# Kernel optimization log

Measured on AMD Instinct MI355X. Metric: run time of the kernel, lower is better.

Reference implementation:

```python
import jax, jax.numpy as jnp
import numpy as np

B, N, D = 8, 500, 256
H, W = 480, 640
NUM_CORNERS = 500
MATCH_RADIUS = 1.0
SCORE_RADIUS = 8
BETA = (1.0, 1.0, 1.0)


def _rodrigues(aa):
    theta = jnp.linalg.norm(aa, axis=-1, keepdims=True)
    k = aa / jnp.maximum(theta, 1e-8)
    kx, ky, kz = k[..., 0], k[..., 1], k[..., 2]
    z = jnp.zeros_like(kx)
    Km = jnp.stack([jnp.stack([z, -kz, ky], -1),
                    jnp.stack([kz, z, -kx], -1),
                    jnp.stack([-ky, kx, z], -1)], -2)
    th = theta[..., None]
    return jnp.eye(3) + jnp.sin(th) * Km + (1. - jnp.cos(th)) * (Km @ Km)


def setup_inputs() -> dict:
    key = jax.random.key(0)
    ks = jax.random.split(key, 8)
    descriptors = jax.random.normal(ks[0], (B, N, D), jnp.float32)
    points = jax.random.uniform(ks[1], (B, N, 2), jnp.float32, -1.0, 1.0)
    pointness = jax.random.uniform(ks[2], (B, 1, H, W), jnp.float32) * 0.98 + 0.01
    depths_dense = jax.random.uniform(ks[3], (B, 1, H, W), jnp.float32) * 4.0 + 1.0
    imgs = jax.random.uniform(ks[4], (B, 3, H, W), jnp.float32)
    aa = jax.random.normal(ks[5], (B, 3), jnp.float32) * 0.02
    t = jax.random.normal(ks[6], (B, 3), jnp.float32) * 0.05
    R = _rodrigues(aa)
    poses = jnp.tile(jnp.eye(4, dtype=jnp.float32), (B, 1, 1))
    poses = poses.at[:, :3, :3].set(R).at[:, :3, 3].set(t)
    Kmat = jnp.tile(jnp.array([[300., 0., W / 2.], [0., 300., H / 2.], [0., 0., 1.]], jnp.float32), (B, 1, 1))
    return {"descriptors": descriptors, "points": points, "pointness": pointness,
            "depths_dense": depths_dense, "poses": poses, "K": Kmat, "imgs": imgs}


def denormalize(pts, h, w):
    return jnp.stack([(pts[..., 0] + 1.) * 0.5 * (w - 1), (pts[..., 1] + 1.) * 0.5 * (h - 1)], -1)


def normalize_pix(pts, h, w):
    return jnp.stack([2. * pts[..., 0] / (w - 1) - 1., 2. * pts[..., 1] / (h - 1) - 1.], -1)


def bilinear_sample(img, px):  # img (H,W), px (...,2) pixel coords
    x = jnp.clip(px[..., 0], 0., W - 1.)
    y = jnp.clip(px[..., 1], 0., H - 1.)
    x0 = jnp.floor(x); y0 = jnp.floor(y)
    x1 = jnp.minimum(x0 + 1., W - 1.); y1 = jnp.minimum(y0 + 1., H - 1.)
    wx = x - x0; wy = y - y0
    x0i = x0.astype(jnp.int32); x1i = x1.astype(jnp.int32)
    y0i = y0.astype(jnp.int32); y1i = y1.astype(jnp.int32)
    v00 = img[y0i, x0i]; v01 = img[y0i, x1i]
    v10 = img[y1i, x0i]; v11 = img[y1i, x1i]
    return v00 * (1 - wx) * (1 - wy) + v01 * wx * (1 - wy) + v10 * (1 - wx) * wy + v11 * wx * wy


def pairwise_project(pts, depths, poses, Kmat):
    # pts (B,N,2) normalized; proj[i,j] = points of frame i projected into frame j
    px = denormalize(pts, H, W)
    d = jax.vmap(bilinear_sample)(depths[:, 0], px)  # (B,Np)
    Kinv = jnp.linalg.inv(Kmat)
    homog = jnp.concatenate([px, jnp.ones_like(px[..., :1])], -1)
    Xc = d[..., None] * jnp.einsum('bij,bnj->bni', Kinv, homog)
    Rm = poses[:, :3, :3]; t = poses[:, :3, 3]
    Xw = jnp.einsum('bij,bnj->bni', Rm, Xc) + t[:, None, :]
    diff = Xw[:, None, :, :] - t[None, :, None, :]           # (src,dst,Np,3)
    Xj = jnp.einsum('jba,ijnb->ijna', Rm, diff)              # R_j^T (Xw - t_j)
    uvw = jnp.einsum('jab,ijnb->ijna', Kmat, Xj)
    z = uvw[..., 2]
    zs = jnp.where(jnp.abs(z) < 1e-6, 1e-6, z)
    pn = normalize_pix(jnp.stack([uvw[..., 0] / zs, uvw[..., 1] / zs], -1), H, W)
    invis = (z <= 1e-6) | (jnp.abs(pn[..., 0]) > 1.) | (jnp.abs(pn[..., 1]) > 1.) | (d[:, None, :] <= 0.)
    return pn, invis


def conv2d_same(x, k):
    return jax.lax.conv_general_dilated(x, k[None, None].astype(x.dtype), (1, 1), 'SAME')


_SOBEL_X = np.array([[-1, 0, 1], [-2, 0, 2], [-1, 0, 1]], np.float32) / 8.


def _gauss_kernel(size=7, sigma=1.0):
    r = np.arange(size) - size // 2
    g = np.exp(-r ** 2 / (2 * sigma ** 2)); g /= g.sum()
    return np.outer(g, g).astype(np.float32)


_GAUSS = _gauss_kernel()


def gftt_response(gray):  # min-eigenvalue (Shi-Tomasi) corner response
    gx = conv2d_same(gray, jnp.asarray(_SOBEL_X))
    gy = conv2d_same(gray, jnp.asarray(_SOBEL_X.T))
    g = jnp.asarray(_GAUSS)
    dx2 = conv2d_same(gx * gx, g)
    dy2 = conv2d_same(gy * gy, g)
    dxy = conv2d_same(gx * gy, g)
    tr = dx2 + dy2
    det = dx2 * dy2 - dxy * dxy
    return 0.5 * (tr - jnp.sqrt(jnp.clip(tr * tr - 4. * det, 0.)))


def nms2d(x, k=5):
    mp = jax.lax.reduce_window(x, -jnp.inf, jax.lax.max, (1, 1, k, k), (1, 1, 1, 1), 'SAME')
    return x * (x == mp).astype(x.dtype)


def get_corners(imgs, depths, poses, Kmat):
    gray = (0.299 * imgs[:, 0] + 0.587 * imgs[:, 1] + 0.114 * imgs[:, 2])[:, None]
    c = nms2d(gftt_response(gray))
    r = SCORE_RADIUS
    blocks = c.reshape(B, 1, H // r, r, W // r, r)  # unfold/fold with stride==kernel
    bm = blocks.max(axis=(3, 5), keepdims=True)
    blocks = blocks * ((blocks > 0) & (blocks == bm)).astype(c.dtype)
    c = blocks.reshape(B, 1, H, W)
    vals, idx = jax.lax.top_k(c.reshape(B, -1), NUM_CORNERS)
    xs = (idx % W).astype(jnp.float32)
    ys = (idx // W).astype(jnp.float32)
    coords = normalize_pix(jnp.stack([xs, ys], -1), H, W)
    proj, invis = pairwise_project(coords, depths, poses, Kmat)
    proj = jnp.where(invis[..., None], -2.0, proj)
    combined = jnp.transpose(proj, (1, 0, 2, 3)).reshape(B, B * NUM_CORNERS, 2)  # per dst frame
    pix = jnp.round(denormalize(combined, H, W)).astype(jnp.int32)
    wq, hq = pix[..., 0], pix[..., 1]
    valid = wq >= 0
    v = jnp.tile(vals.reshape(-1), B).reshape(B, B * NUM_CORNERS)
    v = jnp.where(valid, v, 0.)
    hc = jnp.clip(hq, 0, H - 1)
    wc = jnp.clip(wq, 0, W - 1)
    bidx = jnp.broadcast_to(jnp.arange(B)[:, None], (B, B * NUM_CORNERS))
    target = jnp.zeros((B, H, W), imgs.dtype).at[bidx, hc, wc].max(v)
    target = nms2d(target[:, None])
    return (target > 0).astype(imgs.dtype)


def distinction_loss(desc):
    dn = desc / jnp.clip(jnp.linalg.norm(desc, axis=-1, keepdims=True), 1e-8)
    c = jnp.einsum('bnd,bmd->bnm', dn, dn)
    return jax.nn.relu(c).mean()


def match_loss(desc, points, proj, invis):
    p_src = denormalize(jax.lax.stop_gradient(points), H, W)  # (B,N,2)
    p_dst = denormalize(jax.lax.stop_gradient(proj), H, W)    # (src a, dst b, N, 2)
    diff = p_src[None, :, :, None, :] - p_dst[:, :, None, :, :]  # (a,b,n,m,2)
    m = (diff ** 2).sum(-1) <= MATCH_RADIUS ** 2
    m = m & (~invis)[:, :, :, None]                 # zero invisible rows
    n_idx = jnp.arange(N)
    m = m & (n_idx[:, None] < n_idx[None, :])       # triu(diagonal=1)
    dn = desc / jnp.clip(jnp.linalg.norm(desc, axis=-1, keepdims=True), 1e-8)
    cos = jnp.einsum('bnd,amd->abnm', dn, dn)       # cosine(desc[b,n], desc[a,m])
    mf = m.astype(desc.dtype)
    cnt = jnp.maximum(mf.sum(), 1.)
    return ((1. - cos) * mf).sum() / cnt


def bce(p, t):
    logp = jnp.maximum(jnp.log(p), -100.)
    log1p = jnp.maximum(jnp.log(1. - p), -100.)
    return -(t * logp + (1. - t) * log1p).mean()


def reference(descriptors, points, pointness, depths_dense, poses, K, imgs):
    distinction = distinction_loss(descriptors)
    target = get_corners(imgs, depths_dense, poses, K)
    cornerness = bce(pointness, target)
    proj, invis = pairwise_project(points, depths_dense, poses, K)
    match = match_loss(descriptors, points, proj, invis)
    return BETA[0] * distinction + BETA[1] * cornerness + BETA[2] * match
```

## Files before the change

kernel.cpp:

```cpp
#include <hip/hip_runtime.h>
#include <math.h>

#define BB 8
#define NN 500
#define DDIM 256
#define HH 480
#define WW 640
#define HWSZ (HH*WW)
#define BHW (BB*HWSZ)
#define NBLK 4800
#define NOVF 3392
#define NLIST (BB*NN*BB)
#define NBCE2 512
#define NCORR 125
#define NDM 66

#define PD_DIST  0
#define PD_MS    512
#define PD_MC    1024
#define PD_BCE   1536
#define PD_CORR  2560
#define PD_TOTAL 2688

typedef __attribute__((ext_vector_type(8))) short short8;
typedef __attribute__((ext_vector_type(4))) float f32x4;


static __device__ __forceinline__ float wredmaxf(float v) {
  #pragma unroll
  for (int o = 1; o < 64; o <<= 1) v = fmaxf(v, __shfl_xor(v, o, 64));
  return v;
}

static __device__ __forceinline__ double blockRedSum256(double v) {
  __shared__ double sp[4];
  __syncthreads();
  #pragma unroll
  for (int o = 32; o > 0; o >>= 1) v += __shfl_down(v, o, 64);
  int lane = threadIdx.x & 63, wid = threadIdx.x >> 6;
  if (lane == 0) sp[wid] = v;
  __syncthreads();
  double r = 0.0;
  if (threadIdx.x == 0) r = sp[0] + sp[1] + sp[2] + sp[3];
  return r;
}

static __device__ __forceinline__ unsigned short f2bf(float f) {
  unsigned u = __float_as_uint(f);
  return (unsigned short)((u + 0x7FFFu + ((u >> 16) & 1u)) >> 16);
}

static __device__ __forceinline__ float bilin(const float* __restrict__ img, float px, float py) {
  float x = fminf(fmaxf(px, 0.0f), 639.0f);
  float y = fminf(fmaxf(py, 0.0f), 479.0f);
  float x0 = floorf(x), y0 = floorf(y);
  float x1 = fminf(x0 + 1.0f, 639.0f);
  float y1 = fminf(y0 + 1.0f, 479.0f);
  float wx = x - x0, wy = y - y0;
  int x0i = (int)x0, x1i = (int)x1, y0i = (int)y0, y1i = (int)y1;
  float v00 = img[y0i*WW + x0i], v01 = img[y0i*WW + x1i];
  float v10 = img[y1i*WW + x0i], v11 = img[y1i*WW + x1i];
  return v00*(1.0f-wx)*(1.0f-wy) + v01*wx*(1.0f-wy) + v10*(1.0f-wx)*wy + v11*wx*wy;
}

static __device__ void src_compute(float px, float py, const float* __restrict__ dep,
                                   const float* __restrict__ poses, const float* __restrict__ Km,
                                   int bimg, float* Xw, float* dout) {
  float d = bilin(dep, px, py);
  const float* Kb = Km + bimg*9;
  double a00=Kb[0],a01=Kb[1],a02=Kb[2],a10=Kb[3],a11=Kb[4],a12=Kb[5],a20=Kb[6],a21=Kb[7],a22=Kb[8];
  double det = a00*(a11*a22-a12*a21) - a01*(a10*a22-a12*a20) + a02*(a10*a21-a11*a20);
  double id = 1.0/det;
  float i00=(float)((a11*a22-a12*a21)*id), i01=(float)((a02*a21-a01*a22)*id), i02=(float)((a01*a12-a02*a11)*id);
  float i10=(float)((a12*a20-a10*a22)*id), i11=(float)((a00*a22-a02*a20)*id), i12=(float)((a02*a10-a00*a12)*id);
  float i20=(float)((a10*a21-a11*a20)*id), i21=(float)((a01*a20-a00*a21)*id), i22=(float)((a00*a11-a01*a10)*id);
  float c0 = i00*px + i01*py + i02;
  float c1 = i10*px + i11*py + i12;
  float c2 = i20*px + i21*py + i22;
  float X0 = d*c0, X1 = d*c1, X2 = d*c2;
  const float* P = poses + bimg*16;
  Xw[0] = (P[0]*X0 + P[1]*X1 + P[2]*X2)  + P[3];
  Xw[1] = (P[4]*X0 + P[5]*X1 + P[6]*X2)  + P[7];
  Xw[2] = (P[8]*X0 + P[9]*X1 + P[10]*X2) + P[11];
  *dout = d;
}

static __device__ void project_to(const float* __restrict__ poses, const float* __restrict__ Km,
                                  int j, const float* Xw, float dsrc,
                                  float* pnx, float* pny, bool* invis) {
  const float* P = poses + j*16;
  float d0 = Xw[0]-P[3], d1 = Xw[1]-P[7], d2 = Xw[2]-P[11];
  float Xj0 = P[0]*d0 + P[4]*d1 + P[8]*d2;
  float Xj1 = P[1]*d0 + P[5]*d1 + P[9]*d2;
  float Xj2 = P[2]*d0 + P[6]*d1 + P[10]*d2;
  const float* Kb = Km + j*9;
  float u = Kb[0]*Xj0 + Kb[1]*Xj1 + Kb[2]*Xj2;
  float v = Kb[3]*Xj0 + Kb[4]*Xj1 + Kb[5]*Xj2;
  float z = Kb[6]*Xj0 + Kb[7]*Xj1 + Kb[8]*Xj2;
  float zs = (fabsf(z) < 1e-6f) ? 1e-6f : z;
  float pu = u/zs, pv = v/zs;
  float nx = 2.0f*pu/639.0f - 1.0f;
  float ny = 2.0f*pv/479.0f - 1.0f;
  *pnx = nx; *pny = ny;
  *invis = (z <= 1e-6f) || (fabsf(nx) > 1.0f) || (fabsf(ny) > 1.0f) || (dsrc <= 0.0f);
}


__global__ __launch_bounds__(256) void k_gfused(const float* __restrict__ imgs, float* __restrict__ resp,
                                                int* __restrict__ ovf, int* __restrict__ list,
                                                unsigned int* __restrict__ dnb_u) {
  __shared__ float smem[6536];
  __shared__ float Gw[7];
  float* sgxy = smem;
  float* gray = smem + 2888;
  float* hxx  = smem + 2888;
  float* hyy  = hxx + 1216;
  float* hxy  = hyy + 1216;
  int bx = blockIdx.x*32, by = blockIdx.y*32, b = blockIdx.z;
  int tid = threadIdx.x;
  if (blockIdx.z == 0 && blockIdx.y == 0) {
    int g = blockIdx.x*256 + tid;
    for (int e = g; e < BB*64; e += 20*256) ovf[e] = 0;
    for (int e = g; e < NLIST; e += 20*256) list[e] = -1;
    for (int e = g; e < 12288; e += 20*256) {
      int bi = e / 1536, r = e % 1536;
      dnb_u[(bi*512 + 500)*128 + r] = 0u;
    }
  }
  if (tid < 7) {
    double g[7]; double s = 0.0;
    for (int q = 0; q < 7; q++) { double r = (double)(q-3); g[q] = exp(-(r*r)/2.0); s += g[q]; }
    Gw[tid] = (float)(g[tid]/s);
  }
  const float* ib = imgs + (size_t)b*3*HWSZ;
  for (int e = tid; e < 40*40; e += 256) {
    int ly = e/40, lx = e%40;
    int X = bx - 4 + lx, Y = by - 4 + ly;
    float v = 0.f;
    if (X>=0 && X<WW && Y>=0 && Y<HH) {
      int p = Y*WW + X;
      v = 0.299f*ib[p] + 0.587f*ib[HWSZ+p] + 0.114f*ib[2*HWSZ+p];
    }
    gray[ly*41+lx] = v;
  }
  __syncthreads();
  const float kxw[3][3] = {{-0.125f,0.f,0.125f},{-0.25f,0.f,0.25f},{-0.125f,0.f,0.125f}};
  for (int e = tid; e < 38*38; e += 256) {
    int rr = e/38, c = e%38;
    int X = bx - 3 + c, Y = by - 3 + rr;
    float sx = 0.f, sy = 0.f;
    #pragma unroll
    for (int i = 0; i < 3; i++)
      #pragma unroll
      for (int j = 0; j < 3; j++) {
        float v = gray[(rr+i)*41 + (c+j)];
        sx += kxw[i][j]*v;
        sy += kxw[j][i]*v;
      }
    bool in = (X>=0 && X<WW && Y>=0 && Y<HH);
    sgxy[e*2]   = in ? sx : 0.f;
    sgxy[e*2+1] = in ? sy : 0.f;
  }
  __syncthreads();
  for (int e = tid; e < 38*32; e += 256) {
    int rr = e >> 5, co = e & 31;
    int base = (rr*38 + co)*2;
    float axx = 0.f, ayy = 0.f, axy = 0.f;
    #pragma unroll
    for (int j = 0; j < 7; j++) {
      float a = sgxy[base + j*2];
      float c = sgxy[base + j*2 + 1];
      float Gj = Gw[j];
      axx += Gj*(a*a); ayy += Gj*(c*c); axy += Gj*(a*c);
    }
    hxx[e] = axx; hyy[e] = ayy; hxy[e] = axy;
  }
  __syncthreads();
  int tx = tid & 31, ty = tid >> 5;
  int r0 = ty*4;
  float axx[4] = {0,0,0,0}, ayy[4] = {0,0,0,0}, axy[4] = {0,0,0,0};
  #pragma unroll
  for (int rr = 0; rr < 10; rr++) {
    int r = r0 + rr;
    float vxx = hxx[r*32+tx], vyy = hyy[r*32+tx], vxy = hxy[r*32+tx];
    #pragma unroll
    for (int o = 0; o < 4; o++) {
      int i = rr - o;
      if (i >= 0 && i <= 6) {
        float Gi = Gw[i];
        axx[o] += Gi*vxx; ayy[o] += Gi*vyy; axy[o] += Gi*vxy;
      }
    }
  }
  #pragma unroll
  for (int o = 0; o < 4; o++) {
    float tr = axx[o] + ayy[o];
    float det = axx[o]*ayy[o] - axy[o]*axy[o];
    float disc = fmaxf(tr*tr - 4.0f*det, 0.f);
    int y = by + r0 + o;
    resp[(size_t)b*HWSZ + y*WW + (bx+tx)] = 0.5f*(tr - sqrtf(disc));
  }
}

__global__ __launch_bounds__(256) void k_nmscand(const float* __restrict__ resp, float* __restrict__ cv,
                          int* __restrict__ ci, float* __restrict__ cvo,
                          int* __restrict__ cio, int* __restrict__ ovf,
                          float* __restrict__ target) {
  __shared__ float s[36*37];
  __shared__ float hm[36*32];
  __shared__ float c32[32*32];
  int bx = blockIdx.x*32, by = blockIdx.y*32, b = blockIdx.z;
  int tid = threadIdx.x;
  const float* r = resp + (size_t)b*HWSZ;
  for (int e = tid; e < 36*36; e += 256) {
    int ly = e/36, lx = e%36;
    int X = bx - 2 + lx, Y = by - 2 + ly;
    s[ly*37+lx] = (X>=0 && X<WW && Y>=0 && Y<HH) ? r[Y*WW+X] : -INFINITY;
  }
  __syncthreads();
  for (int e = tid; e < 36*32; e += 256) {
    int rr = e >> 5, co = e & 31;
    int base = rr*37 + co;
    float m = s[base];
    m = fmaxf(m, s[base+1]); m = fmaxf(m, s[base+2]);
    m = fmaxf(m, s[base+3]); m = fmaxf(m, s[base+4]);
    hm[e] = m;
  }
  __syncthreads();
  for (int e = tid; e < 1024; e += 256) {
    int y = e >> 5, x = e & 31;
    float mp = hm[y*32+x];
    mp = fmaxf(mp, hm[(y+1)*32+x]); mp = fmaxf(mp, hm[(y+2)*32+x]);
    mp = fmaxf(mp, hm[(y+3)*32+x]); mp = fmaxf(mp, hm[(y+4)*32+x]);
    float v = s[(y+2)*37 + (x+2)];
    c32[e] = (v == mp) ? v : 0.f;
    target[(size_t)b*HWSZ + (by+y)*WW + (bx+x)] = 0.f;
  }
  __syncthreads();
  int wv = tid >> 6, lane = tid & 63;
  int ly8 = lane >> 3, lx8 = lane & 7;
  for (int q = 0; q < 4; q++) {
    int bb = wv*4 + q;
    int oy = (bb >> 2)*8, ox = (bb & 3)*8;
    float cval = c32[(oy+ly8)*32 + ox+lx8];
    float bm = wredmaxf(cval);
    bool win = (cval > 0.f) && (cval == bm);
    unsigned long long mask = __ballot(win);
    int BY = blockIdx.y*4 + (bb >> 2), BX = blockIdx.x*4 + (bb & 3);
    int rblk = BY*80 + BX;
    int gidx = (by+oy+ly8)*WW + (bx+ox+lx8);
    if (mask == 0ull) {
      if (lane == 0) { cv[b*NBLK+rblk] = 0.f; ci[b*NBLK+rblk] = 0; }
    } else if (win) {
      int rank = __popcll(mask & ((1ull << lane) - 1ull));
      if (rank == 0) { cv[b*NBLK+rblk] = cval; ci[b*NBLK+rblk] = gidx; }
      else {
        int pos = atomicAdd(&ovf[b*64], 1);
        if (pos < NOVF) { cvo[b*NOVF+pos] = cval; cio[b*NOVF+pos] = gidx; }
      }
    }
  }
}

__global__ __launch_bounds__(1024) void k_topscat(const float* __restrict__ cv, const int* __restrict__ ci,
                                                  const float* __restrict__ cvo, const int* __restrict__ cio,
                                                  const int* __restrict__ ovf,
                                                  const float* __restrict__ depths, const float* __restrict__ poses,
                                                  const float* __restrict__ Km,
                                                  unsigned int* __restrict__ target, int* __restrict__ list) {
  __shared__ unsigned int hist[256];
  __shared__ unsigned long long prefix_s;
  __shared__ int kk_s, fin_s, cgt_s, ceq_s;
  __shared__ float s_topv[NN];
  __shared__ int s_topi[NN];
  int b = blockIdx.x;
  int tid = threadIdx.x;
  int nval = min(ovf[b*64], NOVF);
  unsigned long long kreg[8];
  #pragma unroll
  for (int q = 0; q < 8; q++) {
    int e = tid + q*1024;
    float v = 0.f; unsigned int idx = 0u;
    if (e < NBLK) { v = cv[b*NBLK+e]; idx = (unsigned int)ci[b*NBLK+e]; }
    else if (e - NBLK < nval) { v = cvo[b*NOVF+e-NBLK]; idx = (unsigned int)cio[b*NOVF+e-NBLK]; }
    kreg[q] = ((unsigned long long)__float_as_uint(v) << 32) | (0xFFFFFFFFu - idx);
  }
  if (tid == 0) { prefix_s = 0ull; kk_s = NN; fin_s = -1; cgt_s = 0; ceq_s = 0; }
  if (tid < 256) hist[tid] = 0u;
  __syncthreads();
  for (int round = 0; round < 8; round++) {
    int shift = 56 - 8*round;
    unsigned long long prefix = prefix_s;
    int kk = kk_s;
    unsigned long long himask = (round == 0) ? 0ull : (~0ull << (shift + 8));
    #pragma unroll
    for (int q = 0; q < 8; q++)
      if ((kreg[q] & himask) == prefix)
        atomicAdd(&hist[(unsigned int)((kreg[q] >> shift) & 255ull)], 1u);
    __syncthreads();
    if (tid < 64) {
      int l = tid;
      unsigned s0 = hist[l], s1 = hist[64+l], s2 = hist[128+l], s3 = hist[192+l];
      #pragma unroll
      for (int off = 1; off < 64; off <<= 1) {
        unsigned t0 = __shfl_down(s0, off, 64), t1 = __shfl_down(s1, off, 64);
        unsigned t2 = __shfl_down(s2, off, 64), t3 = __shfl_down(s3, off, 64);
        if (l + off < 64) { s0 += t0; s1 += t1; s2 += t2; s3 += t3; }
      }
      unsigned S1 = __shfl(s1, 0, 64), S2 = __shfl(s2, 0, 64), S3 = __shfl(s3, 0, 64);
      unsigned suf0 = s0 + S1 + S2 + S3, suf1 = s1 + S2 + S3, suf2 = s2 + S3, suf3 = s3;
      int best = -1;
      if      (suf3 >= (unsigned)kk) best = 192 + l;
      else if (suf2 >= (unsigned)kk) best = 128 + l;
      else if (suf1 >= (unsigned)kk) best = 64 + l;
      else if (suf0 >= (unsigned)kk) best = l;
      #pragma unroll
      for (int off = 1; off < 64; off <<= 1) best = max(best, __shfl_xor(best, off, 64));
      if (l == (best & 63)) {
        int seg = best >> 6;
        unsigned sufb = (seg == 3) ? suf3 : ((seg == 2) ? suf2 : ((seg == 1) ? suf1 : suf0));
        unsigned c = hist[best];
        int Sn = (int)(sufb - c);
        int kkn = kk - Sn;
        prefix_s = prefix | ((unsigned long long)best << shift);
        kk_s = kkn;
        if (kkn == (int)c) fin_s = shift;
      }
      hist[l] = 0u; hist[64+l] = 0u; hist[128+l] = 0u; hist[192+l] = 0u;
    }
    __syncthreads();
    if (fin_s >= 0) break;
  }
  int sg = (fin_s > 0) ? fin_s : 0;
  unsigned long long prefix = prefix_s;
  int kk = kk_s;
  unsigned long long low = (sg > 0) ? ((1ull << sg) - 1ull) : 0ull;
  unsigned long long Tfull = prefix | low;
  unsigned long long mhi = ~low;
  #pragma unroll
  for (int q = 0; q < 8; q++) {
    unsigned long long key = kreg[q];
    int slot = -1;
    if (key > Tfull) slot = atomicAdd(&cgt_s, 1);
    else if ((key & mhi) == prefix) {
      int p = atomicAdd(&ceq_s, 1);
      if (p < kk) slot = (NN-1) - p;
    }
    if (slot >= 0) {
      s_topv[slot] = __uint_as_float((unsigned int)(key >> 32));
      s_topi[slot] = (int)(0xFFFFFFFFu - (unsigned int)(key & 0xFFFFFFFFull));
    }
  }
  __syncthreads();
  if (tid < NN) {
    float val = s_topv[tid];
    if (val > 0.f) {
      int idx = s_topi[tid];
      float xs = (float)(idx % WW), ys = (float)(idx / WW);
      float cx = 2.0f*xs/639.0f - 1.0f;
      float cy = 2.0f*ys/479.0f - 1.0f;
      float px = (cx + 1.0f)*0.5f*639.0f;
      float py = (cy + 1.0f)*0.5f*479.0f;
      float Xw[3], d;
      src_compute(px, py, depths + (size_t)b*HWSZ, poses, Km, b, Xw, &d);
      int tglob = b*NN + tid;
      for (int j = 0; j < BB; j++) {
        float nx, ny; bool inv;
        project_to(poses, Km, j, Xw, d, &nx, &ny, &inv);
        if (inv) { nx = -2.0f; ny = -2.0f; }
        float fx = rintf((nx + 1.0f)*0.5f*639.0f);
        float fy = rintf((ny + 1.0f)*0.5f*479.0f);
        int wq = (int)fx, hq = (int)fy;
        if (wq < 0) continue;
        int hc = min(max(hq, 0), HH-1), wc = min(max(wq, 0), WW-1);
        int p = j*HWSZ + hc*WW + wc;
        unsigned int old = atomicMax(&target[p], __float_as_uint(val));
        if (old == 0u) list[tglob*BB + j] = p;
      }
    }
  }
}

__global__ __launch_bounds__(256) void k_misc(const float* __restrict__ desc, float* __restrict__ dn,
                                              unsigned short* __restrict__ dnb,
                                              const float* __restrict__ points, const float* __restrict__ depths,
                                              const float* __restrict__ poses, const float* __restrict__ Km,
                                              float* __restrict__ psrc, float* __restrict__ pdst, int* __restrict__ minv,
                                              const float* __restrict__ pn, const int* __restrict__ list,
                                              const float* __restrict__ target, double* __restrict__ pd) {
  int bid = blockIdx.x, tid = threadIdx.x;
  if (bid < 4000) {
    int row = bid;
    float v = desc[(size_t)row*DDIM + tid];
    __shared__ float sp2[4];
    __shared__ float den_s;
    float s = v*v;
    #pragma unroll
    for (int o = 32; o > 0; o >>= 1) s += __shfl_down(s, o, 64);
    int lane = tid & 63, wid = tid >> 6;
    if (lane == 0) sp2[wid] = s;
    __syncthreads();
    if (tid == 0) den_s = fmaxf(sqrtf(sp2[0]+sp2[1]+sp2[2]+sp2[3]), 1e-8f);
    __syncthreads();
    float o = v / den_s;
    dn[(size_t)row*DDIM + tid] = o;
    int pr = (row/500)*512 + (row%500);
    dnb[(size_t)pr*DDIM + tid] = f2bf(o);
  } else if (bid < 4016) {
    int t = (bid - 4000)*256 + tid;
    if (t < BB*NN) {
      int a = t / NN, m = t % NN;
      float p0 = points[t*2], p1 = points[t*2+1];
      float px = (p0 + 1.0f)*0.5f*639.0f;
      float py = (p1 + 1.0f)*0.5f*479.0f;
      float Xw[3], d;
      src_compute(px, py, depths + (size_t)a*HWSZ, poses, Km, a, Xw, &d);
      psrc[t*2] = px; psrc[t*2+1] = py;
      for (int b = 0; b < BB; b++) {
        float nx, ny; bool inv;
        project_to(poses, Km, b, Xw, d, &nx, &ny, &inv);
        int o = (a*BB + b)*NN + m;
        pdst[o*2]   = (nx + 1.0f)*0.5f*639.0f;
        pdst[o*2+1] = (ny + 1.0f)*0.5f*479.0f;
        minv[o] = inv ? 1 : 0;
      }
    }
  } else if (bid < 4016 + NBCE2) {
    int blk = bid - 4016;
    int g = blk*256 + tid;
    double l = 0.0;
    for (int q = g; q < BHW/4; q += NBCE2*256) {
      float4 v = ((const float4*)pn)[q];
      l -= (double)fmaxf(logf(1.f - v.x), -100.f);
      l -= (double)fmaxf(logf(1.f - v.y), -100.f);
      l -= (double)fmaxf(logf(1.f - v.z), -100.f);
      l -= (double)fmaxf(logf(1.f - v.w), -100.f);
    }
    double s = blockRedSum256(l);
    if (tid == 0) pd[PD_BCE + blk] = s;
  } else {
    int blk = bid - (4016 + NBCE2);
    int g = blk*256 + tid;
    double l = 0.0;
    if (g < NLIST) {
      int p = list[g];
      if (p >= 0) {
        int j = p / HWSZ, pix = p % HWSZ;
        int y = pix / WW, x = pix % WW;
        const float* tb = target + (size_t)j*HWSZ;
        float v = tb[pix];
        float mp = -INFINITY;
        for (int dy = -2; dy <= 2; dy++) {
          int yy = y + dy; if (yy < 0 || yy >= HH) continue;
          for (int dx = -2; dx <= 2; dx++) {
            int xx = x + dx; if (xx < 0 || xx >= WW) continue;
            mp = fmaxf(mp, tb[yy*WW+xx]);
          }
        }
        if (v > 0.f && v == mp) {
          float pv = pn[p];
          l = (double)(-fmaxf(logf(pv), -100.f)) + (double)fmaxf(logf(1.f - pv), -100.f);
        }
      }
    }
    double s = blockRedSum256(l);
    if (tid == 0) pd[PD_CORR + blk] = s;
  }
}

__global__ __launch_bounds__(256) void k_tail(const float* __restrict__ psrc, const float* __restrict__ pdst,
                                              const int* __restrict__ minv, const float* __restrict__ dn,
                                              const short* __restrict__ dnb, double* __restrict__ pd) {
  __shared__ float sbuf[2500];
  int bid = blockIdx.x, tid = threadIdx.x;
  if (bid < NDM) {
    int w = tid >> 6, lane = tid & 63;
    int gw = bid*4 + w;
    int r16 = lane & 15, koff = (lane >> 4)*8;
    double dsum = 0.0;
    for (int j = 0; j < 16; j++) {
      int jb = gw*16 + j;
      int b = jb / 528, t = jb % 528;
      int I = (int)((sqrtf(8.f*(float)t + 1.f) - 1.f)*0.5f);
      while ((I+1)*(I+2)/2 <= t) I++;
      while (I*(I+1)/2 > t) I--;
      int J = t - I*(I+1)/2;
      const short* bp = dnb + (size_t)b*512*DDIM;
      const short* ap = bp + (I*16 + r16)*DDIM + koff;
      const short* cp = bp + (J*16 + r16)*DDIM + koff;
      f32x4 acc = {0.f, 0.f, 0.f, 0.f};
      #pragma unroll
      for (int kk = 0; kk < 8; kk++) {
        short8 af = *(const short8*)(ap + kk*32);
        short8 bf = *(const short8*)(cp + kk*32);
        acc = __builtin_amdgcn_mfma_f32_16x16x32_bf16(af, bf, acc, 0, 0, 0);
      }
      float ls = fmaxf(acc[0],0.f) + fmaxf(acc[1],0.f) + fmaxf(acc[2],0.f) + fmaxf(acc[3],0.f);
      dsum += (double)ls * ((I == J) ? 1.0 : 2.0);
    }
    double s = blockRedSum256(dsum);
    if (tid == 0) pd[PD_DIST + bid] = s;
  } else {
    int mbid = bid - NDM;
    float* spd = sbuf;
    float* ssrc = sbuf + 1000;
    int* sinv = (int*)(sbuf + 2000);
    int ab = mbid & 63; int b = ab % BB; int a = ab / BB;
    int ys = mbid >> 6;
    for (int e = tid; e < NN; e += 256) {
      spd[e*2]   = pdst[(ab*NN+e)*2];
      spd[e*2+1] = pdst[(ab*NN+e)*2+1];
      sinv[e]    = minv[ab*NN+e];
      ssrc[e*2]   = psrc[(b*NN+e)*2];
      ssrc[e*2+1] = psrc[(b*NN+e)*2+1];
    }
    __syncthreads();
    double lsum = 0.0, lcnt = 0.0;
    for (int mm = ys; mm < NN; mm += 8) {
      float px = spd[mm*2], py = spd[mm*2+1];
      for (int nn = tid; nn < mm; nn += 256) {
        if (sinv[nn]) continue;
        float dx = ssrc[nn*2]   - px;
        float dy = ssrc[nn*2+1] - py;
        if (dx*dx + dy*dy <= 1.0f) {
          const float* da = dn + ((size_t)a*NN + mm)*DDIM;
          const float* db = dn + ((size_t)b*NN + nn)*DDIM;
          float dot = 0.f;
          for (int q = 0; q < DDIM; q++) dot += db[q]*da[q];
          lsum += (double)(1.0f - dot);
          lcnt += 1.0;
        }
      }
    }
    double s = blockRedSum256(lsum);
    if (tid == 0) pd[PD_MS + mbid] = s;
    double c2 = blockRedSum256(lcnt);
    if (tid == 0) pd[PD_MC + mbid] = c2;
  }
}

__global__ void k_final(const double* __restrict__ pd, float* __restrict__ out) {
  int tid = threadIdx.x;
  double l;
  l = 0.0; for (int i = tid; i < NDM;   i += 256) l += pd[PD_DIST + i];
  double dist = blockRedSum256(l);
  l = 0.0; for (int i = tid; i < 512;   i += 256) l += pd[PD_MS + i];
  double ms = blockRedSum256(l);
  l = 0.0; for (int i = tid; i < 512;   i += 256) l += pd[PD_MC + i];
  double mc = blockRedSum256(l);
  l = 0.0; for (int i = tid; i < NBCE2; i += 256) l += pd[PD_BCE + i];
  double bce = blockRedSum256(l);
  l = 0.0; for (int i = tid; i < NCORR; i += 256) l += pd[PD_CORR + i];
  double corr = blockRedSum256(l);
  if (tid == 0) {
    float distf = (float)(dist / (double)(BB*NN*NN));
    float cornf = (float)((bce + corr) / (double)BHW);
    float cntf  = fmaxf((float)mc, 1.0f);
    float matchf = (float)ms / cntf;
    out[0] = distf + cornf + matchf;
  }
}


extern "C" void kernel_launch(void* const* d_in, const int* in_sizes, int n_in,
                              void* d_out, int out_size, void* d_ws, size_t ws_size,
                              hipStream_t stream) {
  (void)in_sizes; (void)n_in; (void)out_size; (void)ws_size;
  const float* desc      = (const float*)d_in[0];
  const float* points    = (const float*)d_in[1];
  const float* pointness = (const float*)d_in[2];
  const float* depths    = (const float*)d_in[3];
  const float* poses     = (const float*)d_in[4];
  const float* Kmat      = (const float*)d_in[5];
  const float* imgs      = (const float*)d_in[6];
  float* out = (float*)d_out;

  double* pd = (double*)d_ws;
  float* f = (float*)(pd + PD_TOTAL);
  float* bufA = f;
  float* bufC = bufA + (size_t)BHW;
  float* cv_main = bufC + (size_t)BHW;
  int*   ci_main = (int*)(cv_main + BB*NBLK);
  float* cv_ovf  = (float*)(ci_main + BB*NBLK);
  int*   ci_ovf  = (int*)(cv_ovf + BB*NOVF);
  int*   ovf     = (int*)(ci_ovf + BB*NOVF);
  float* psrc = (float*)(ovf + BB*64);
  float* pdst = psrc + BB*NN*2;
  int*   minv = (int*)(pdst + BB*BB*NN*2);
  float* dn   = (float*)(minv + BB*BB*NN);
  int*   list = (int*)(dn + (size_t)BB*NN*DDIM);
  unsigned short* dnb = (unsigned short*)(list + NLIST);

  dim3 tgrid(WW/32, HH/32, BB);

  k_gfused <<<tgrid, 256, 0, stream>>>(imgs, bufA, ovf, list, (unsigned int*)dnb);
  k_nmscand<<<tgrid, 256, 0, stream>>>(bufA, cv_main, ci_main, cv_ovf, ci_ovf, ovf, bufC);
  k_topscat<<<BB, 1024, 0, stream>>>(cv_main, ci_main, cv_ovf, ci_ovf, ovf,
                                     depths, poses, Kmat, (unsigned int*)bufC, list);
  k_misc   <<<4016 + NBCE2 + NCORR, 256, 0, stream>>>(desc, dn, dnb, points, depths, poses, Kmat,
                                                      psrc, pdst, minv, pointness, list, bufC, pd);
  k_tail   <<<NDM + 512, 256, 0, stream>>>(psrc, pdst, minv, dn, (const short*)dnb, pd);
  k_final  <<<1, 256, 0, stream>>>(pd, out);
}
```

Before: 124.7 us.

## Merge independent work into front kernel and privatize top-k histograms

Moves descriptor normalization, point projection and the dense BCE reduction, which do not depend on the corner pipeline, into the first kernel alongside the Harris response blocks. The corner-correction pass moves into the tail kernel, so k_misc and one launch go away. In top-k selection the radix histogram is split into per-wavefront copies to reduce shared atomic contention, and slot assignment uses wave-aggregated ballot atomics. The cost is extra shared-memory clearing and summing each round, and a larger mixed-role front kernel whose block roles may balance unevenly.

```diff
diff --git a/kernel.cpp b/kernel.cpp
--- a/kernel.cpp
+++ b/kernel.cpp
@@ -106,99 +106,158 @@
 }
 
 
-__global__ __launch_bounds__(256) void k_gfused(const float* __restrict__ imgs, float* __restrict__ resp,
-                                                int* __restrict__ ovf, int* __restrict__ list,
-                                                unsigned int* __restrict__ dnb_u) {
+__global__ __launch_bounds__(256) void k_front(const float* __restrict__ imgs, float* __restrict__ resp,
+                                               int* __restrict__ ovf, int* __restrict__ list,
+                                               unsigned int* __restrict__ dnb_u,
+                                               const float* __restrict__ desc, float* __restrict__ dn,
+                                               unsigned short* __restrict__ dnb,
+                                               const float* __restrict__ points, const float* __restrict__ depths,
+                                               const float* __restrict__ poses, const float* __restrict__ Km,
+                                               float* __restrict__ psrc, float* __restrict__ pdst,
+                                               int* __restrict__ minv,
+                                               const float* __restrict__ pn, double* __restrict__ pd) {
   __shared__ float smem[6536];
   __shared__ float Gw[7];
-  float* sgxy = smem;
-  float* gray = smem + 2888;
-  float* hxx  = smem + 2888;
-  float* hyy  = hxx + 1216;
-  float* hxy  = hyy + 1216;
-  int bx = blockIdx.x*32, by = blockIdx.y*32, b = blockIdx.z;
-  int tid = threadIdx.x;
-  if (blockIdx.z == 0 && blockIdx.y == 0) {
-    int g = blockIdx.x*256 + tid;
-    for (int e = g; e < BB*64; e += 20*256) ovf[e] = 0;
-    for (int e = g; e < NLIST; e += 20*256) list[e] = -1;
-    for (int e = g; e < 12288; e += 20*256) {
-      int bi = e / 1536, r = e % 1536;
-      dnb_u[(bi*512 + 500)*128 + r] = 0u;
-    }
-  }
-  if (tid < 7) {
-    double g[7]; double s = 0.0;
-    for (int q = 0; q < 7; q++) { double r = (double)(q-3); g[q] = exp(-(r*r)/2.0); s += g[q]; }
-    Gw[tid] = (float)(g[tid]/s);
-  }
-  const float* ib = imgs + (size_t)b*3*HWSZ;
-  for (int e = tid; e < 40*40; e += 256) {
-    int ly = e/40, lx = e%40;
-    int X = bx - 4 + lx, Y = by - 4 + ly;
-    float v = 0.f;
-    if (X>=0 && X<WW && Y>=0 && Y<HH) {
-      int p = Y*WW + X;
-      v = 0.299f*ib[p] + 0.587f*ib[HWSZ+p] + 0.114f*ib[2*HWSZ+p];
-    }
-    gray[ly*41+lx] = v;
-  }
-  __syncthreads();
-  const float kxw[3][3] = {{-0.125f,0.f,0.125f},{-0.25f,0.f,0.25f},{-0.125f,0.f,0.125f}};
-  for (int e = tid; e < 38*38; e += 256) {
-    int rr = e/38, c = e%38;
-    int X = bx - 3 + c, Y = by - 3 + rr;
-    float sx = 0.f, sy = 0.f;
+  int bid = blockIdx.x, tid = threadIdx.x;
+  if (bid < 2400) {
+    float* sgxy = smem;
+    float* gray = smem + 2888;
+    float* hxx  = smem + 2888;
+    float* hyy  = hxx + 1216;
+    float* hxy  = hyy + 1216;
+    int b = bid / 300, r = bid % 300;
+    int byi = r / 20, bxi = r % 20;
+    int bx = bxi*32, by = byi*32;
+    if (bid < 20) {
+      int g = bid*256 + tid;
+      for (int e = g; e < BB*64; e += 20*256) ovf[e] = 0;
+      for (int e = g; e < NLIST; e += 20*256) list[e] = -1;
+      for (int e = g; e < 12288; e += 20*256) {
+        int bi = e / 1536, rr2 = e % 1536;
+        dnb_u[(bi*512 + 500)*128 + rr2] = 0u;
+      }
+    }
+    if (tid < 7) {
+      double g[7]; double s = 0.0;
+      for (int q = 0; q < 7; q++) { double rr2 = (double)(q-3); g[q] = exp(-(rr2*rr2)/2.0); s += g[q]; }
+      Gw[tid] = (float)(g[tid]/s);
+    }
+    const float* ib = imgs + (size_t)b*3*HWSZ;
+    for (int e = tid; e < 40*40; e += 256) {
+      int ly = e/40, lx = e%40;
+      int X = bx - 4 + lx, Y = by - 4 + ly;
+      float v = 0.f;
+      if (X>=0 && X<WW && Y>=0 && Y<HH) {
+        int p = Y*WW + X;
+        v = 0.299f*ib[p] + 0.587f*ib[HWSZ+p] + 0.114f*ib[2*HWSZ+p];
+      }
+      gray[ly*41+lx] = v;
+    }
+    __syncthreads();
+    const float kxw[3][3] = {{-0.125f,0.f,0.125f},{-0.25f,0.f,0.25f},{-0.125f,0.f,0.125f}};
+    for (int e = tid; e < 38*38; e += 256) {
+      int rr2 = e/38, c = e%38;
+      int X = bx - 3 + c, Y = by - 3 + rr2;
+      float sx = 0.f, sy = 0.f;
+      #pragma unroll
+      for (int i = 0; i < 3; i++)
+        #pragma unroll
+        for (int j = 0; j < 3; j++) {
+          float v = gray[(rr2+i)*41 + (c+j)];
+          sx += kxw[i][j]*v;
+          sy += kxw[j][i]*v;
+        }
+      bool in = (X>=0 && X<WW && Y>=0 && Y<HH);
+      sgxy[e*2]   = in ? sx : 0.f;
+      sgxy[e*2+1] = in ? sy : 0.f;
+    }
+    __syncthreads();
+    for (int e = tid; e < 38*32; e += 256) {
+      int rr2 = e >> 5, co = e & 31;
+      int base = (rr2*38 + co)*2;
+      float axx = 0.f, ayy = 0.f, axy = 0.f;
+      #pragma unroll
+      for (int j = 0; j < 7; j++) {
+        float a = sgxy[base + j*2];
+        float c = sgxy[base + j*2 + 1];
+        float Gj = Gw[j];
+        axx += Gj*(a*a); ayy += Gj*(c*c); axy += Gj*(a*c);
+      }
+      hxx[e] = axx; hyy[e] = ayy; hxy[e] = axy;
+    }
+    __syncthreads();
+    int tx = tid & 31, ty = tid >> 5;
+    int r0 = ty*4;
+    float axx[4] = {0,0,0,0}, ayy[4] = {0,0,0,0}, axy[4] = {0,0,0,0};
     #pragma unroll
-    for (int i = 0; i < 3; i++)
+    for (int rr2 = 0; rr2 < 10; rr2++) {
+      int rr3 = r0 + rr2;
+      float vxx = hxx[rr3*32+tx], vyy = hyy[rr3*32+tx], vxy = hxy[rr3*32+tx];
       #pragma unroll
-      for (int j = 0; j < 3; j++) {
-        float v = gray[(rr+i)*41 + (c+j)];
-        sx += kxw[i][j]*v;
-        sy += kxw[j][i]*v;
-      }
-    bool in = (X>=0 && X<WW && Y>=0 && Y<HH);
-    sgxy[e*2]   = in ? sx : 0.f;
-    sgxy[e*2+1] = in ? sy : 0.f;
-  }
-  __syncthreads();
-  for (int e = tid; e < 38*32; e += 256) {
-    int rr = e >> 5, co = e & 31;
-    int base = (rr*38 + co)*2;
-    float axx = 0.f, ayy = 0.f, axy = 0.f;
-    #pragma unroll
-    for (int j = 0; j < 7; j++) {
-      float a = sgxy[base + j*2];
-      float c = sgxy[base + j*2 + 1];
-      float Gj = Gw[j];
-      axx += Gj*(a*a); ayy += Gj*(c*c); axy += Gj*(a*c);
-    }
-    hxx[e] = axx; hyy[e] = ayy; hxy[e] = axy;
-  }
-  __syncthreads();
-  int tx = tid & 31, ty = tid >> 5;
-  int r0 = ty*4;
-  float axx[4] = {0,0,0,0}, ayy[4] = {0,0,0,0}, axy[4] = {0,0,0,0};
-  #pragma unroll
-  for (int rr = 0; rr < 10; rr++) {
-    int r = r0 + rr;
-    float vxx = hxx[r*32+tx], vyy = hyy[r*32+tx], vxy = hxy[r*32+tx];
+      for (int o = 0; o < 4; o++) {
+        int i = rr2 - o;
+        if (i >= 0 && i <= 6) {
+          float Gi = Gw[i];
+          axx[o] += Gi*vxx; ayy[o] += Gi*vyy; axy[o] += Gi*vxy;
+        }
+      }
+    }
     #pragma unroll
     for (int o = 0; o < 4; o++) {
-      int i = rr - o;
-      if (i >= 0 && i <= 6) {
-        float Gi = Gw[i];
-        axx[o] += Gi*vxx; ayy[o] += Gi*vyy; axy[o] += Gi*vxy;
-      }
-    }
-  }
-  #pragma unroll
-  for (int o = 0; o < 4; o++) {
-    float tr = axx[o] + ayy[o];
-    float det = axx[o]*ayy[o] - axy[o]*axy[o];
-    float disc = fmaxf(tr*tr - 4.0f*det, 0.f);
-    int y = by + r0 + o;
-    resp[(size_t)b*HWSZ + y*WW + (bx+tx)] = 0.5f*(tr - sqrtf(disc));
+      float tr = axx[o] + ayy[o];
+      float det = axx[o]*ayy[o] - axy[o]*axy[o];
+      float disc = fmaxf(tr*tr - 4.0f*det, 0.f);
+      int y = by + r0 + o;
+      resp[(size_t)b*HWSZ + y*WW + (bx+tx)] = 0.5f*(tr - sqrtf(disc));
+    }
+  } else if (bid < 6400) {
+    int row = bid - 2400;
+    float v = desc[(size_t)row*DDIM + tid];
+    float* sp2 = smem;
+    float s = v*v;
+    #pragma unroll
+    for (int o = 32; o > 0; o >>= 1) s += __shfl_down(s, o, 64);
+    int lane = tid & 63, wid = tid >> 6;
+    if (lane == 0) sp2[wid] = s;
+    __syncthreads();
+    if (tid == 0) sp2[4] = fmaxf(sqrtf(sp2[0]+sp2[1]+sp2[2]+sp2[3]), 1e-8f);
+    __syncthreads();
+    float o = v / sp2[4];
+    dn[(size_t)row*DDIM + tid] = o;
+    int pr = (row/500)*512 + (row%500);
+    dnb[(size_t)pr*DDIM + tid] = f2bf(o);
+  } else if (bid < 6416) {
+    int t = (bid - 6400)*256 + tid;
+    if (t < BB*NN) {
+      int a = t / NN, m = t % NN;
+      float p0 = points[t*2], p1 = points[t*2+1];
+      float px = (p0 + 1.0f)*0.5f*639.0f;
+      float py = (p1 + 1.0f)*0.5f*479.0f;
+      float Xw[3], d;
+      src_compute(px, py, depths + (size_t)a*HWSZ, poses, Km, a, Xw, &d);
+      psrc[t*2] = px; psrc[t*2+1] = py;
+      for (int b = 0; b < BB; b++) {
+        float nx, ny; bool inv;
+        project_to(poses, Km, b, Xw, d, &nx, &ny, &inv);
+        int o = (a*BB + b)*NN + m;
+        pdst[o*2]   = (nx + 1.0f)*0.5f*639.0f;
+        pdst[o*2+1] = (ny + 1.0f)*0.5f*479.0f;
+        minv[o] = inv ? 1 : 0;
+      }
+    }
+  } else {
+    int blk = bid - 6416;
+    int g = blk*256 + tid;
+    double l = 0.0;
+    for (int q = g; q < BHW/4; q += NBCE2*256) {
+      float4 v = ((const float4*)pn)[q];
+      l -= (double)fmaxf(logf(1.f - v.x), -100.f);
+      l -= (double)fmaxf(logf(1.f - v.y), -100.f);
+      l -= (double)fmaxf(logf(1.f - v.z), -100.f);
+      l -= (double)fmaxf(logf(1.f - v.w), -100.f);
+    }
+    double s = blockRedSum256(l);
+    if (tid == 0) pd[PD_BCE + blk] = s;
   }
 }
 
@@ -268,13 +327,15 @@
                                                   const float* __restrict__ depths, const float* __restrict__ poses,
                                                   const float* __restrict__ Km,
                                                   unsigned int* __restrict__ target, int* __restrict__ list) {
-  __shared__ unsigned int hist[256];
+  __shared__ unsigned int hist[16*257];
+  __shared__ unsigned int histsum[256];
   __shared__ unsigned long long prefix_s;
   __shared__ int kk_s, fin_s, cgt_s, ceq_s;
   __shared__ float s_topv[NN];
   __shared__ int s_topi[NN];
   int b = blockIdx.x;
   int tid = threadIdx.x;
+  int w257 = (tid >> 6)*257;
   int nval = min(ovf[b*64], NOVF);
   unsigned long long kreg[8];
   #pragma unroll
@@ -286,7 +347,7 @@
     kreg[q] = ((unsigned long long)__float_as_uint(v) << 32) | (0xFFFFFFFFu - idx);
   }
   if (tid == 0) { prefix_s = 0ull; kk_s = NN; fin_s = -1; cgt_s = 0; ceq_s = 0; }
-  if (tid < 256) hist[tid] = 0u;
+  for (int e = tid; e < 16*257; e += 1024) hist[e] = 0u;
   __syncthreads();
   for (int round = 0; round < 8; round++) {
     int shift = 56 - 8*round;
@@ -296,11 +357,19 @@
     #pragma unroll
     for (int q = 0; q < 8; q++)
       if ((kreg[q] & himask) == prefix)
-        atomicAdd(&hist[(unsigned int)((kreg[q] >> shift) & 255ull)], 1u);
-    __syncthreads();
+        atomicAdd(&hist[w257 + (unsigned int)((kreg[q] >> shift) & 255ull)], 1u);
+    __syncthreads();
+    if (tid < 256) {
+      unsigned s = 0u;
+      #pragma unroll
+      for (int ww = 0; ww < 16; ww++) s += hist[ww*257 + tid];
+      histsum[tid] = s;
+    }
+    __syncthreads();
+    for (int e = tid; e < 16*257; e += 1024) hist[e] = 0u;
     if (tid < 64) {
       int l = tid;
-      unsigned s0 = hist[l], s1 = hist[64+l], s2 = hist[128+l], s3 = hist[192+l];
+      unsigned s0 = histsum[l], s1 = histsum[64+l], s2 = histsum[128+l], s3 = histsum[192+l];
       #pragma unroll
       for (int off = 1; off < 64; off <<= 1) {
         unsigned t0 = __shfl_down(s0, off, 64), t1 = __shfl_down(s1, off, 64);
@@ -319,14 +388,13 @@
       if (l == (best & 63)) {
         int seg = best >> 6;
         unsigned sufb = (seg == 3) ? suf3 : ((seg == 2) ? suf2 : ((seg == 1) ? suf1 : suf0));
-        unsigned c = hist[best];
+        unsigned c = histsum[best];
         int Sn = (int)(sufb - c);
         int kkn = kk - Sn;
         prefix_s = prefix | ((unsigned long long)best << shift);
         kk_s = kkn;
         if (kkn == (int)c) fin_s = shift;
       }
-      hist[l] = 0u; hist[64+l] = 0u; hist[128+l] = 0u; hist[192+l] = 0u;
     }
     __syncthreads();
     if (fin_s >= 0) break;
@@ -337,14 +405,32 @@
   unsigned long long low = (sg > 0) ? ((1ull << sg) - 1ull) : 0ull;
   unsigned long long Tfull = prefix | low;
   unsigned long long mhi = ~low;
+  int lane = tid & 63;
+  unsigned long long lmask = (1ull << lane) - 1ull;
   #pragma unroll
   for (int q = 0; q < 8; q++) {
     unsigned long long key = kreg[q];
+    bool gt = key > Tfull;
+    bool eq = !gt && ((key & mhi) == prefix);
+    unsigned long long mg = __ballot(gt);
+    unsigned long long me = __ballot(eq);
     int slot = -1;
-    if (key > Tfull) slot = atomicAdd(&cgt_s, 1);
-    else if ((key & mhi) == prefix) {
-      int p = atomicAdd(&ceq_s, 1);
-      if (p < kk) slot = (NN-1) - p;
+    if (mg != 0ull) {
+      int ldr = __ffsll((long long)mg) - 1;
+      int baseg = 0;
+      if (lane == ldr) baseg = atomicAdd(&cgt_s, (int)__popcll(mg));
+      baseg = __shfl(baseg, ldr, 64);
+      if (gt) slot = baseg + (int)__popcll(mg & lmask);
+    }
+    if (me != 0ull) {
+      int ldr = __ffsll((long long)me) - 1;
+      int basee = 0;
+      if (lane == ldr) basee = atomicAdd(&ceq_s, (int)__popcll(me));
+      basee = __shfl(basee, ldr, 64);
+      if (eq) {
+        int p = basee + (int)__popcll(me & lmask);
+        if (p < kk) slot = (NN-1) - p;
+      }
     }
     if (slot >= 0) {
       s_topv[slot] = __uint_as_float((unsigned int)(key >> 32));
@@ -381,96 +467,11 @@
   }
 }
 
-__global__ __launch_bounds__(256) void k_misc(const float* __restrict__ desc, float* __restrict__ dn,
-                                              unsigned short* __restrict__ dnb,
-                                              const float* __restrict__ points, const float* __restrict__ depths,
-                                              const float* __restrict__ poses, const float* __restrict__ Km,
-                                              float* __restrict__ psrc, float* __restrict__ pdst, int* __restrict__ minv,
-                                              const float* __restrict__ pn, const int* __restrict__ list,
-                                              const float* __restrict__ target, double* __restrict__ pd) {
-  int bid = blockIdx.x, tid = threadIdx.x;
-  if (bid < 4000) {
-    int row = bid;
-    float v = desc[(size_t)row*DDIM + tid];
-    __shared__ float sp2[4];
-    __shared__ float den_s;
-    float s = v*v;
-    #pragma unroll
-    for (int o = 32; o > 0; o >>= 1) s += __shfl_down(s, o, 64);
-    int lane = tid & 63, wid = tid >> 6;
-    if (lane == 0) sp2[wid] = s;
-    __syncthreads();
-    if (tid == 0) den_s = fmaxf(sqrtf(sp2[0]+sp2[1]+sp2[2]+sp2[3]), 1e-8f);
-    __syncthreads();
-    float o = v / den_s;
-    dn[(size_t)row*DDIM + tid] = o;
-    int pr = (row/500)*512 + (row%500);
-    dnb[(size_t)pr*DDIM + tid] = f2bf(o);
-  } else if (bid < 4016) {
-    int t = (bid - 4000)*256 + tid;
-    if (t < BB*NN) {
-      int a = t / NN, m = t % NN;
-      float p0 = points[t*2], p1 = points[t*2+1];
-      float px = (p0 + 1.0f)*0.5f*639.0f;
-      float py = (p1 + 1.0f)*0.5f*479.0f;
-      float Xw[3], d;
-      src_compute(px, py, depths + (size_t)a*HWSZ, poses, Km, a, Xw, &d);
-      psrc[t*2] = px; psrc[t*2+1] = py;
-      for (int b = 0; b < BB; b++) {
-        float nx, ny; bool inv;
-        project_to(poses, Km, b, Xw, d, &nx, &ny, &inv);
-        int o = (a*BB + b)*NN + m;
-        pdst[o*2]   = (nx + 1.0f)*0.5f*639.0f;
-        pdst[o*2+1] = (ny + 1.0f)*0.5f*479.0f;
-        minv[o] = inv ? 1 : 0;
-      }
-    }
-  } else if (bid < 4016 + NBCE2) {
-    int blk = bid - 4016;
-    int g = blk*256 + tid;
-    double l = 0.0;
-    for (int q = g; q < BHW/4; q += NBCE2*256) {
-      float4 v = ((const float4*)pn)[q];
-      l -= (double)fmaxf(logf(1.f - v.x), -100.f);
-      l -= (double)fmaxf(logf(1.f - v.y), -100.f);
-      l -= (double)fmaxf(logf(1.f - v.z), -100.f);
-      l -= (double)fmaxf(logf(1.f - v.w), -100.f);
-    }
-    double s = blockRedSum256(l);
-    if (tid == 0) pd[PD_BCE + blk] = s;
-  } else {
-    int blk = bid - (4016 + NBCE2);
-    int g = blk*256 + tid;
-    double l = 0.0;
-    if (g < NLIST) {
-      int p = list[g];
-      if (p >= 0) {
-        int j = p / HWSZ, pix = p % HWSZ;
-        int y = pix / WW, x = pix % WW;
-        const float* tb = target + (size_t)j*HWSZ;
-        float v = tb[pix];
-        float mp = -INFINITY;
-        for (int dy = -2; dy <= 2; dy++) {
-          int yy = y + dy; if (yy < 0 || yy >= HH) continue;
-          for (int dx = -2; dx <= 2; dx++) {
-            int xx = x + dx; if (xx < 0 || xx >= WW) continue;
-            mp = fmaxf(mp, tb[yy*WW+xx]);
-          }
-        }
-        if (v > 0.f && v == mp) {
-          float pv = pn[p];
-          l = (double)(-fmaxf(logf(pv), -100.f)) + (double)fmaxf(logf(1.f - pv), -100.f);
-        }
-      }
-    }
-    double s = blockRedSum256(l);
-    if (tid == 0) pd[PD_CORR + blk] = s;
-  }
-}
-
 __global__ __launch_bounds__(256) void k_tail(const float* __restrict__ psrc, const float* __restrict__ pdst,
                                               const int* __restrict__ minv, const float* __restrict__ dn,
-                                              const short* __restrict__ dnb, double* __restrict__ pd) {
+                                              const short* __restrict__ dnb,
+                                              const int* __restrict__ list, const float* __restrict__ target,
+                                              const float* __restrict__ pn, double* __restrict__ pd) {
   __shared__ float sbuf[2500];
   int bid = blockIdx.x, tid = threadIdx.x;
   if (bid < NDM) {
@@ -500,7 +501,7 @@
     }
     double s = blockRedSum256(dsum);
     if (tid == 0) pd[PD_DIST + bid] = s;
-  } else {
+  } else if (bid < NDM + 512) {
     int mbid = bid - NDM;
     float* spd = sbuf;
     float* ssrc = sbuf + 1000;
@@ -536,6 +537,33 @@
     if (tid == 0) pd[PD_MS + mbid] = s;
     double c2 = blockRedSum256(lcnt);
     if (tid == 0) pd[PD_MC + mbid] = c2;
+  } else {
+    int blk = bid - (NDM + 512);
+    int g = blk*256 + tid;
+    double l = 0.0;
+    if (g < NLIST) {
+      int p = list[g];
+      if (p >= 0) {
+        int j = p / HWSZ, pix = p % HWSZ;
+        int y = pix / WW, x = pix % WW;
+        const float* tb = target + (size_t)j*HWSZ;
+        float v = tb[pix];
+        float mp = -INFINITY;
+        for (int dy = -2; dy <= 2; dy++) {
+          int yy = y + dy; if (yy < 0 || yy >= HH) continue;
+          for (int dx = -2; dx <= 2; dx++) {
+            int xx = x + dx; if (xx < 0 || xx >= WW) continue;
+            mp = fmaxf(mp, tb[yy*WW+xx]);
+          }
+        }
+        if (v > 0.f && v == mp) {
+          float pv = pn[p];
+          l = (double)(-fmaxf(logf(pv), -100.f)) + (double)fmaxf(logf(1.f - pv), -100.f);
+        }
+      }
+    }
+    double s = blockRedSum256(l);
+    if (tid == 0) pd[PD_CORR + blk] = s;
   }
 }
 
@@ -593,12 +621,13 @@
 
   dim3 tgrid(WW/32, HH/32, BB);
 
-  k_gfused <<<tgrid, 256, 0, stream>>>(imgs, bufA, ovf, list, (unsigned int*)dnb);
+  k_front  <<<6928, 256, 0, stream>>>(imgs, bufA, ovf, list, (unsigned int*)dnb,
+                                      desc, dn, dnb, points, depths, poses, Kmat,
+                                      psrc, pdst, minv, pointness, pd);
   k_nmscand<<<tgrid, 256, 0, stream>>>(bufA, cv_main, ci_main, cv_ovf, ci_ovf, ovf, bufC);
   k_topscat<<<BB, 1024, 0, stream>>>(cv_main, ci_main, cv_ovf, ci_ovf, ovf,
                                      depths, poses, Kmat, (unsigned int*)bufC, list);
-  k_misc   <<<4016 + NBCE2 + NCORR, 256, 0, stream>>>(desc, dn, dnb, points, depths, poses, Kmat,
-                                                      psrc, pdst, minv, pointness, list, bufC, pd);
-  k_tail   <<<NDM + 512, 256, 0, stream>>>(psrc, pdst, minv, dn, (const short*)dnb, pd);
+  k_tail   <<<NDM + 512 + NCORR, 256, 0, stream>>>(psrc, pdst, minv, dn, (const short*)dnb,
+                                                   list, bufC, pointness, pd);
   k_final  <<<1, 256, 0, stream>>>(pd, out);
 }
```

After: 110.4 us. 11.5% less time.
